# Kernel optimization log

Hardware: AMD Instinct MI355X
Metric: run time of the kernel (lower is better)

The kernel has to match this reference:

```python
import jax, jax.numpy as jnp
import numpy as np


def _conv2d(x, w, b, padding):
    # x: [N,C,H,W], w: [O,I,kh,kw]
    y = jax.lax.conv_general_dilated(
        x, w, window_strides=(1, 1), padding=padding,
        dimension_numbers=("NCHW", "OIHW", "NCHW"))
    return y + b[None, :, None, None]


def setup_inputs() -> dict:
    key = jax.random.key(0)
    ks = jax.random.split(key, 9)
    s = 0.05
    return {
        "x": jax.random.normal(ks[0], (16, 4, 512, 512), dtype=jnp.float32),
        "w1": jax.random.normal(ks[1], (32, 4, 3, 3), dtype=jnp.float32) * s,
        "b1": jax.random.normal(ks[2], (32,), dtype=jnp.float32) * s,
        "w2": jax.random.normal(ks[3], (4, 32, 3, 3), dtype=jnp.float32) * s,
        "b2": jax.random.normal(ks[4], (4,), dtype=jnp.float32) * s,
        "w_se1": jax.random.normal(ks[5], (16, 32, 1, 1), dtype=jnp.float32) * s,
        "b_se1": jax.random.normal(ks[6], (16,), dtype=jnp.float32) * s,
        "w_se2": jax.random.normal(ks[7], (32, 16, 1, 1), dtype=jnp.float32) * s,
        "b_se2": jax.random.normal(ks[8], (32,), dtype=jnp.float32) * s,
    }


def reference(x, w1, b1, w2, b2, w_se1, b_se1, w_se2, b_se2):
    x1 = x
    # module1: 3x3 conv (4->32) + ReLU
    h = jax.nn.relu(_conv2d(x, w1, b1, padding="SAME"))  # [N,32,H,W]
    se_in = h
    # SE branch: global avg pool -> 1x1 conv -> ReLU -> 1x1 conv -> sigmoid
    p = jnp.mean(h, axis=(2, 3), keepdims=True)  # [N,32,1,1]
    p = jax.nn.relu(_conv2d(p, w_se1, b_se1, padding="VALID"))  # [N,16,1,1]
    p = jax.nn.sigmoid(_conv2d(p, w_se2, b_se2, padding="VALID"))  # [N,32,1,1]
    h = p * se_in  # broadcast channel scaling
    # module2: 3x3 conv (32->4) + ReLU
    h = jax.nn.relu(_conv2d(h, w2, b2, padding="SAME"))  # [N,4,H,W]
    return h * x1  # residual multiply
```

## Files before the change

kernel.cpp:

```cpp
#include <hip/hip_runtime.h>
#include <math.h>

#define IMG 512

typedef __attribute__((ext_vector_type(4))) short short4_t;
typedef __attribute__((ext_vector_type(8))) short short8;
typedef __attribute__((ext_vector_type(4))) float f32x4;
typedef __attribute__((ext_vector_type(16))) float f32x16;
typedef __attribute__((ext_vector_type(2))) unsigned int u32x2;

__device__ __forceinline__ unsigned short f2bf(float f) {
  unsigned u = __builtin_bit_cast(unsigned, f);
  u += 0x7FFFu + ((u >> 16) & 1u);
  return (unsigned short)(u >> 16);
}
__device__ __forceinline__ unsigned cvtpk(float lo, float hi) {
  unsigned r;
  asm("v_cvt_pk_bf16_f32 %0, %1, %2" : "=v"(r) : "v"(lo), "v"(hi));
  return r;
}

__global__ __launch_bounds__(256) void k_prep(const float* __restrict__ w1,
                                              unsigned short* __restrict__ w1f) {
  const int t = threadIdx.x;
  if (t < 192) {
    const int kk = t >> 6, lane = t & 63;
    const int oc = lane & 31, hi = lane >> 5;
#pragma unroll
    for (int j = 0; j < 8; ++j) {
      const int dxp = 2 * hi + (j >> 2), ic = j & 3;
      float v = (dxp < 3) ? w1[((oc * 4 + ic) * 3 + kk) * 3 + dxp] : 0.f;
      w1f[(kk * 64 + lane) * 8 + j] = f2bf(v);
    }
  }
}

__global__ __launch_bounds__(256, 3) void k_pool(
    const float* __restrict__ x, const unsigned short* __restrict__ w1f,
    const float* __restrict__ b1, float* __restrict__ red_out, int use_atomic) {
  __shared__ unsigned short xs[34 * 40 * 4];
  __shared__ float pools[4][2][16];
  const int bid = blockIdx.x;
  const int swz = (bid & 7) * 512 + (bid >> 3);
  const int bx = swz & 15, by = (swz >> 4) & 15, n = swz >> 8;
  const int x0 = bx * 32, y0 = by * 32;
  const int t = threadIdx.x, lane = t & 63, wv = t >> 6;
  const int hi = lane >> 5;

  short8 A1[3];
#pragma unroll
  for (int kk = 0; kk < 3; ++kk)
    A1[kk] = *(const short8*)&w1f[(kk * 64 + lane) * 8];
  float bias_r[16];
#pragma unroll
  for (int r = 0; r < 16; ++r) {
    float bl = b1[(r & 3) + 8 * (r >> 2)], bh = b1[(r & 3) + 8 * (r >> 2) + 4];
    bias_r[r] = hi ? bh : bl;
  }

  const int sx = x0 - 4;
  const long CS = (long)IMG * IMG;
  for (int i = t; i < 340; i += 256) {
    const int row = i / 10, cb = i % 10;
    const int gy = y0 - 1 + row, gx0 = sx + cb * 4;
    f32x4 v0 = {0.f, 0.f, 0.f, 0.f}, v1 = v0, v2 = v0, v3 = v0;
    if (gy >= 0 && gy < IMG && gx0 >= 0 && gx0 < IMG) {
      const float* p = x + (((long)(n * 4) * IMG + gy) * IMG + gx0);
      v0 = *(const f32x4*)p;
      v1 = *(const f32x4*)(p + CS);
      v2 = *(const f32x4*)(p + 2 * CS);
      v3 = *(const f32x4*)(p + 3 * CS);
    }
    unsigned short* d = &xs[(row * 40 + cb * 4) * 4];
#pragma unroll
    for (int j = 0; j < 4; ++j) {
      u32x2 w;
      w[0] = cvtpk(v0[j], v1[j]);
      w[1] = cvtpk(v2[j], v3[j]);
      *(u32x2*)(d + j * 4) = w;
    }
  }
  __syncthreads();

  float pacc[16];
#pragma unroll
  for (int r = 0; r < 16; ++r) pacc[r] = 0.f;
  const int cx0 = (lane & 31) + 2 * hi + 3;
  const unsigned short* pP = &xs[((wv * 8) * 40 + cx0) * 4];
#define LOADP(K)                                                              \
  __builtin_shufflevector(*(const short4_t*)(pP + (K)*160),                   \
                          *(const short4_t*)(pP + (K)*160 + 4), 0, 1, 2, 3,   \
                          4, 5, 6, 7)
  short8 Ba, Bb, Bc;
  Ba = LOADP(0);
  Bb = LOADP(1);
#define P_ITER(IT, B0, B1, B2)                                                \
  {                                                                           \
    B2 = LOADP((IT) + 2);                                                     \
    f32x16 C;                                                                 \
    _Pragma("unroll") for (int r = 0; r < 16; ++r) C[r] = bias_r[r];          \
    C = __builtin_amdgcn_mfma_f32_32x32x16_bf16(A1[0], B0, C, 0, 0, 0);       \
    C = __builtin_amdgcn_mfma_f32_32x32x16_bf16(A1[1], B1, C, 0, 0, 0);       \
    C = __builtin_amdgcn_mfma_f32_32x32x16_bf16(A1[2], B2, C, 0, 0, 0);       \
    _Pragma("unroll") for (int r = 0; r < 16; ++r)                            \
        pacc[r] += fmaxf(C[r], 0.f);                                          \
  }
  P_ITER(0, Ba, Bb, Bc)
  P_ITER(1, Bb, Bc, Ba)
  P_ITER(2, Bc, Ba, Bb)
  P_ITER(3, Ba, Bb, Bc)
  P_ITER(4, Bb, Bc, Ba)
  P_ITER(5, Bc, Ba, Bb)
  P_ITER(6, Ba, Bb, Bc)
  P_ITER(7, Bb, Bc, Ba)
#undef P_ITER
#undef LOADP
#pragma unroll
  for (int r = 0; r < 16; ++r) {
#pragma unroll
    for (int m = 1; m < 32; m <<= 1) pacc[r] += __shfl_xor(pacc[r], m);
  }
  if ((lane & 31) == 0) {
#pragma unroll
    for (int r = 0; r < 16; ++r) pools[wv][hi][r] = pacc[r];
  }
  __syncthreads();
  if (t < 32) {
    const int c = t;
    const int hic = (c >> 2) & 1, reg = (c & 3) + 4 * (c >> 3);
    float s = pools[0][hic][reg] + pools[1][hic][reg] + pools[2][hic][reg] +
              pools[3][hic][reg];
    if (use_atomic) {
      atomicAdd(&red_out[n * 32 + c], s);
    } else {
      red_out[(n * 256 + by * 16 + bx) * 32 + c] = s;
    }
  }
}

__global__ __launch_bounds__(256) void k_se(
    const float* __restrict__ partials, const float* __restrict__ sums,
    const float* __restrict__ w_se1, const float* __restrict__ b_se1,
    const float* __restrict__ w_se2, const float* __restrict__ b_se2,
    const float* __restrict__ w2, unsigned short* __restrict__ w2f, int det) {
  const int n = blockIdx.x, t = threadIdx.x;
  __shared__ float red[8][32];
  __shared__ float mean_s[32], f1[16], p[32];
  if (det) {
    const int c = t & 31, s = t >> 5;
    float a = 0.f;
    for (int i = s * 32; i < s * 32 + 32; ++i)
      a += partials[(n * 256 + i) * 32 + c];
    red[s][c] = a;
    __syncthreads();
    if (t < 32) {
      float v = 0.f;
#pragma unroll
      for (int s2 = 0; s2 < 8; ++s2) v += red[s2][t];
      mean_s[t] = v * (1.0f / (512.f * 512.f));
    }
  } else {
    if (t < 32) mean_s[t] = sums[n * 32 + t] * (1.0f / (512.f * 512.f));
  }
  __syncthreads();
  if (t < 16) {
    float a = b_se1[t];
#pragma unroll
    for (int c = 0; c < 32; ++c) a += w_se1[t * 32 + c] * mean_s[c];
    f1[t] = fmaxf(a, 0.f);
  }
  __syncthreads();
  if (t < 32) {
    float a = b_se2[t];
#pragma unroll
    for (int c = 0; c < 16; ++c) a += w_se2[t * 16 + c] * f1[c];
    p[t] = 1.f / (1.f + expf(-a));
  }
  __syncthreads();
  for (int i = t; i < 9216; i += 256) {
    const int s = i >> 9, rem = i & 511, lane2 = rem >> 3, j = rem & 7;
    const int oc = lane2 & 3, yo = (lane2 >> 2) & 3, cg = lane2 >> 4;
    const int c = cg * 8 + j;
    const int dyy = s / 3, dx = s - dyy * 3, dy = dyy - yo;
    float v = 0.f;
    if (dy >= 0 && dy < 3) v = w2[(oc * 32 + c) * 9 + dy * 3 + dx] * p[c];
    w2f[((n * 18 + s) * 64 + lane2) * 8 + j] = f2bf(v);
  }
}

__global__ __launch_bounds__(256, 3) void k_main(
    const float* __restrict__ x, const unsigned short* __restrict__ w1f,
    const float* __restrict__ b1, const unsigned short* __restrict__ w2f,
    const float* __restrict__ b2, float* __restrict__ out) {
  __shared__ unsigned short xs[20 * 40 * 4];
  __shared__ unsigned short hs[18 * 32 * 32];
  const int bid = blockIdx.x;
  const int swz = (bid & 7) * 1152 + (bid >> 3);
  const int bx = swz % 18;
  const int q = swz / 18;
  const int by = q & 31, n = q >> 5;
  const int x0 = bx * 30, y0 = by * 16;
  const int t = threadIdx.x, lane = t & 63, wv = t >> 6;
  const int hi = lane >> 5;

  short8 A1[3];
#pragma unroll
  for (int kk = 0; kk < 3; ++kk)
    A1[kk] = *(const short8*)&w1f[(kk * 64 + lane) * 8];
  float bias_r[16];
#pragma unroll
  for (int r = 0; r < 16; ++r) {
    float bl = b1[(r & 3) + 8 * (r >> 2)], bh = b1[(r & 3) + 8 * (r >> 2) + 4];
    bias_r[r] = hi ? bh : bl;
  }

  const int sx = (x0 - 4) & ~3;
  const long CS = (long)IMG * IMG;
  for (int i = t; i < 200; i += 256) {
    const int row = i / 10, cb = i % 10;
    const int gy = y0 - 2 + row, gx0 = sx + cb * 4;
    f32x4 v0 = {0.f, 0.f, 0.f, 0.f}, v1 = v0, v2 = v0, v3 = v0;
    if (gy >= 0 && gy < IMG && gx0 >= 0 && gx0 < IMG) {
      const float* p = x + (((long)(n * 4) * IMG + gy) * IMG + gx0);
      v0 = *(const f32x4*)p;
      v1 = *(const f32x4*)(p + CS);
      v2 = *(const f32x4*)(p + 2 * CS);
      v3 = *(const f32x4*)(p + 3 * CS);
    }
    unsigned short* d = &xs[(row * 40 + cb * 4) * 4];
#pragma unroll
    for (int j = 0; j < 4; ++j) {
      u32x2 w;
      w[0] = cvtpk(v0[j], v1[j]);
      w[1] = cvtpk(v2[j], v3[j]);
      *(u32x2*)(d + j * 4) = w;
    }
  }
  __syncthreads();

  {
    const int px = lane & 31;
    const int cx0 = px + 2 * hi + (x0 - 2 - sx);
    const int q2 = (px >> 1) & 3;
    const int gxc = x0 - 1 + px;
    const bool colok = (gxc >= 0) && (gxc < IMG);
    const bool col_int = (x0 >= 1) && (x0 + 30 < IMG);
    const int R0 = (wv < 2) ? wv * 5 : 10 + (wv - 2) * 4;
    const unsigned short* pR = &xs[(R0 * 40 + cx0) * 4];
#define LOADX(K)                                                              \
  __builtin_shufflevector(*(const short4_t*)(pR + (K)*160),                   \
                          *(const short4_t*)(pR + (K)*160 + 4), 0, 1, 2, 3,   \
                          4, 5, 6, 7)
    short8 Ba, Bb, Bc;
    Ba = LOADX(0);
    Bb = LOADX(1);
#define C1_ITER(IT, B0, B1, B2)                                               \
  {                                                                           \
    B2 = LOADX((IT) + 2);                                                     \
    const int hy = R0 + (IT);                                                 \
    const int yi = y0 - 1 + hy;                                               \
    const bool row_ok = (yi >= 0) && (yi < IMG);                              \
    f32x16 C;                                                                 \
    _Pragma("unroll") for (int r = 0; r < 16; ++r) C[r] = bias_r[r];          \
    C = __builtin_amdgcn_mfma_f32_32x32x16_bf16(A1[0], B0, C, 0, 0, 0);       \
    C = __builtin_amdgcn_mfma_f32_32x32x16_bf16(A1[1], B1, C, 0, 0, 0);       \
    C = __builtin_amdgcn_mfma_f32_32x32x16_bf16(A1[2], B2, C, 0, 0, 0);       \
    const int usb = hy * 1024 + px * 32 + (hi << 2);                          \
    if (row_ok && col_int) {                                                  \
      _Pragma("unroll") for (int g = 0; g < 4; ++g) {                         \
        u32x2 w;                                                              \
        w[0] = cvtpk(fmaxf(C[4 * g + 0], 0.f), fmaxf(C[4 * g + 1], 0.f));     \
        w[1] = cvtpk(fmaxf(C[4 * g + 2], 0.f), fmaxf(C[4 * g + 3], 0.f));     \
        *(u32x2*)&hs[usb + ((g ^ q2) << 3)] = w;                              \
      }                                                                       \
    } else if (row_ok) {                                                      \
      _Pragma("unroll") for (int g = 0; g < 4; ++g) {                         \
        unsigned p01 =                                                        \
            cvtpk(fmaxf(C[4 * g + 0], 0.f), fmaxf(C[4 * g + 1], 0.f));        \
        unsigned p23 =                                                        \
            cvtpk(fmaxf(C[4 * g + 2], 0.f), fmaxf(C[4 * g + 3], 0.f));        \
        u32x2 w;                                                              \
        w[0] = colok ? p01 : 0u;                                              \
        w[1] = colok ? p23 : 0u;                                              \
        *(u32x2*)&hs[usb + ((g ^ q2) << 3)] = w;                              \
      }                                                                       \
    } else {                                                                  \
      u32x2 z;                                                                \
      z[0] = 0u;                                                              \
      z[1] = 0u;                                                              \
      _Pragma("unroll") for (int g = 0; g < 4; ++g)                           \
          *(u32x2*)&hs[usb + ((g ^ q2) << 3)] = z;                            \
    }                                                                         \
  }
    C1_ITER(0, Ba, Bb, Bc)
    C1_ITER(1, Bb, Bc, Ba)
    C1_ITER(2, Bc, Ba, Bb)
    C1_ITER(3, Ba, Bb, Bc)
    if (wv < 2) C1_ITER(4, Bb, Bc, Ba)
#undef C1_ITER
#undef LOADX
  }

  const unsigned short* w2b = w2f + (size_t)n * 9216 + lane * 8;
  short8 A2_0 = *(const short8*)(w2b + 0 * 512);
  short8 A2_1 = *(const short8*)(w2b + 1 * 512);
  short8 A2_2 = *(const short8*)(w2b + 2 * 512);
  short8 A2_3 = *(const short8*)(w2b + 3 * 512);
  short8 A2_4 = *(const short8*)(w2b + 4 * 512);
  short8 A2_5 = *(const short8*)(w2b + 5 * 512);
  short8 A2_6 = *(const short8*)(w2b + 6 * 512);
  short8 A2_7 = *(const short8*)(w2b + 7 * 512);
  short8 A2_8 = *(const short8*)(w2b + 8 * 512);
  short8 A2_9 = *(const short8*)(w2b + 9 * 512);
  short8 A2_10 = *(const short8*)(w2b + 10 * 512);
  short8 A2_11 = *(const short8*)(w2b + 11 * 512);
  short8 A2_12 = *(const short8*)(w2b + 12 * 512);
  short8 A2_13 = *(const short8*)(w2b + 13 * 512);
  short8 A2_14 = *(const short8*)(w2b + 14 * 512);
  short8 A2_15 = *(const short8*)(w2b + 15 * 512);
  short8 A2_16 = *(const short8*)(w2b + 16 * 512);
  short8 A2_17 = *(const short8*)(w2b + 17 * 512);
  asm volatile("" ::"v"(A2_0), "v"(A2_1), "v"(A2_2), "v"(A2_3), "v"(A2_4),
               "v"(A2_5), "v"(A2_6), "v"(A2_7), "v"(A2_8), "v"(A2_9),
               "v"(A2_10), "v"(A2_11), "v"(A2_12), "v"(A2_13), "v"(A2_14),
               "v"(A2_15), "v"(A2_16), "v"(A2_17));
  __syncthreads();

  {
    const int px16 = lane & 15, cg = lane >> 4;
    const int grp = wv & 1, ybq = wv >> 1;
    const int ox = grp * 16 + px16;
    const int yo = lane >> 4;
    const int gxo = x0 + ox;
    const bool epi_ok = (ox < 30) && (gxo < IMG);
    const float b20 = b2[0], b21 = b2[1], b22 = b2[2], b23 = b2[3];
    const int n4 = n * 4;
    int ph0 = ox + 0, ph1 = ox + 1, ph2 = ox + 2;
    ph2 = ph2 < 31 ? ph2 : 31;
    ph1 = ph1 < 31 ? ph1 : 31;
    const int ba0 = ph0 * 64 + ((cg ^ ((ph0 >> 1) & 3)) << 4);
    const int ba1 = ph1 * 64 + ((cg ^ ((ph1 >> 1) & 3)) << 4);
    const int ba2 = ph2 * 64 + ((cg ^ ((ph2 >> 1) & 3)) << 4);
    const char* hb = (const char*)hs + (ybq * 8) * 2048;
    f32x4 CA = {b20, b21, b22, b23};
    f32x4 CB = {b20, b21, b22, b23};
    short8 F0, F1, F2;

#define LOADF(R)                                                              \
  F0 = *(const short8*)(hb + (R)*2048 + ba0);                                 \
  F1 = *(const short8*)(hb + (R)*2048 + ba1);                                 \
  F2 = *(const short8*)(hb + (R)*2048 + ba2);
#define MFA(S0, S1, S2)                                                       \
  CA = __builtin_amdgcn_mfma_f32_16x16x32_bf16(A2_##S0, F0, CA, 0, 0, 0);     \
  CA = __builtin_amdgcn_mfma_f32_16x16x32_bf16(A2_##S1, F1, CA, 0, 0, 0);     \
  CA = __builtin_amdgcn_mfma_f32_16x16x32_bf16(A2_##S2, F2, CA, 0, 0, 0);
#define MFB(S0, S1, S2)                                                       \
  CB = __builtin_amdgcn_mfma_f32_16x16x32_bf16(A2_##S0, F0, CB, 0, 0, 0);     \
  CB = __builtin_amdgcn_mfma_f32_16x16x32_bf16(A2_##S1, F1, CB, 0, 0, 0);     \
  CB = __builtin_amdgcn_mfma_f32_16x16x32_bf16(A2_##S2, F2, CB, 0, 0, 0);

    __builtin_amdgcn_s_setprio(1);
    LOADF(0) MFA(0, 1, 2)
    LOADF(1) MFA(3, 4, 5)
    LOADF(2) MFA(6, 7, 8)
    LOADF(3) MFA(9, 10, 11)
    LOADF(4) MFA(12, 13, 14) MFB(0, 1, 2)
    LOADF(5) MFA(15, 16, 17) MFB(3, 4, 5)
    LOADF(6) MFB(6, 7, 8)
    LOADF(7) MFB(9, 10, 11)
    LOADF(8) MFB(12, 13, 14)
    LOADF(9) MFB(15, 16, 17)
    __builtin_amdgcn_s_setprio(0);
#undef LOADF
#undef MFA
#undef MFB

#define EPI2(CV, YB)                                                          \
  if (epi_ok) {                                                               \
    const int gy = y0 + (YB) + yo;                                            \
    const long i0 = ((long)n4 * IMG + gy) * IMG + gxo;                        \
    out[i0] = fmaxf(CV[0], 0.f) * x[i0];                                      \
    out[i0 + CS] = fmaxf(CV[1], 0.f) * x[i0 + CS];                            \
    out[i0 + 2 * CS] = fmaxf(CV[2], 0.f) * x[i0 + 2 * CS];                    \
    out[i0 + 3 * CS] = fmaxf(CV[3], 0.f) * x[i0 + 3 * CS];                    \
  }
    EPI2(CA, ybq * 8)
    EPI2(CB, ybq * 8 + 4)
#undef EPI2
  }
}

extern "C" void kernel_launch(void* const* d_in, const int* in_sizes, int n_in,
                              void* d_out, int out_size, void* d_ws,
                              size_t ws_size, hipStream_t stream) {
  const float* x = (const float*)d_in[0];
  const float* w1 = (const float*)d_in[1];
  const float* b1 = (const float*)d_in[2];
  const float* w2 = (const float*)d_in[3];
  const float* b2 = (const float*)d_in[4];
  const float* w_se1 = (const float*)d_in[5];
  const float* b_se1 = (const float*)d_in[6];
  const float* w_se2 = (const float*)d_in[7];
  const float* b_se2 = (const float*)d_in[8];
  float* out = (float*)d_out;
  float* ws = (float*)d_ws;

  float* sums = ws;
  unsigned short* w1f = (unsigned short*)(ws + 512);
  unsigned short* w2f = w1f + 1536;
  float* partials = (float*)(w2f + 147456);
  const size_t need_full =
      512 * 4 + 1536 * 2 + (size_t)147456 * 2 + (size_t)131072 * 4;

  k_prep<<<1, 256, 0, stream>>>(w1, w1f);
  if (ws_size >= need_full) {
    k_pool<<<4096, 256, 0, stream>>>(x, w1f, b1, partials, 0);
    k_se<<<16, 256, 0, stream>>>(partials, sums, w_se1, b_se1, w_se2, b_se2,
                                 w2, w2f, 1);
  } else {
    hipMemsetAsync(sums, 0, 512 * sizeof(float), stream);
    k_pool<<<4096, 256, 0, stream>>>(x, w1f, b1, sums, 1);
    k_se<<<16, 256, 0, stream>>>(partials, sums, w_se1, b_se1, w_se2, b_se2,
                                 w2, w2f, 0);
  }
  k_main<<<9216, 256, 0, stream>>>(x, w1f, b1, w2f, b2, out);
}
```

Baseline: 102.5 us.

## Process four row tiles per block with double-buffered input staging

Each block of the main fused conv kernel now walks four consecutive 16-row tiles instead of one, and the grid shrinks fourfold. The per-sample conv2 weights and the conv1 weights and biases are loaded once per block and reused across tiles. The x tile for the next rows is loaded into registers while conv1 runs on the current tile, then written to a second LDS buffer, so global load latency overlaps compute. The cost is more LDS (two staging buffers), extra barriers per tile, and fewer blocks to spread across CUs, which may lower occupancy or leave the load unbalanced.

```diff
diff --git a/kernel.cpp b/kernel.cpp
--- a/kernel.cpp
+++ b/kernel.cpp
@@ -8,6 +8,7 @@
 typedef __attribute__((ext_vector_type(4))) float f32x4;
 typedef __attribute__((ext_vector_type(16))) float f32x16;
 typedef __attribute__((ext_vector_type(2))) unsigned int u32x2;
+typedef __attribute__((ext_vector_type(4))) unsigned int u32x4;
 
 __device__ __forceinline__ unsigned short f2bf(float f) {
   unsigned u = __builtin_bit_cast(unsigned, f);
@@ -192,16 +193,43 @@
     const float* __restrict__ x, const unsigned short* __restrict__ w1f,
     const float* __restrict__ b1, const unsigned short* __restrict__ w2f,
     const float* __restrict__ b2, float* __restrict__ out) {
-  __shared__ unsigned short xs[20 * 40 * 4];
+  __shared__ unsigned short xs[2][20 * 40 * 4];
   __shared__ unsigned short hs[18 * 32 * 32];
   const int bid = blockIdx.x;
-  const int swz = (bid & 7) * 1152 + (bid >> 3);
+  const int swz = (bid & 7) * 288 + (bid >> 3);
   const int bx = swz % 18;
   const int q = swz / 18;
-  const int by = q & 31, n = q >> 5;
-  const int x0 = bx * 30, y0 = by * 16;
+  const int byq = q & 7, n = q >> 3;
+  const int x0 = bx * 30;
+  const int ybase = byq * 64;
   const int t = threadIdx.x, lane = t & 63, wv = t >> 6;
   const int hi = lane >> 5;
+  const int n4 = n * 4;
+  const long CS = (long)IMG * IMG;
+
+  const unsigned short* w2b = w2f + (size_t)n * 9216 + lane * 8;
+  short8 A2_0 = *(const short8*)(w2b + 0 * 512);
+  short8 A2_1 = *(const short8*)(w2b + 1 * 512);
+  short8 A2_2 = *(const short8*)(w2b + 2 * 512);
+  short8 A2_3 = *(const short8*)(w2b + 3 * 512);
+  short8 A2_4 = *(const short8*)(w2b + 4 * 512);
+  short8 A2_5 = *(const short8*)(w2b + 5 * 512);
+  short8 A2_6 = *(const short8*)(w2b + 6 * 512);
+  short8 A2_7 = *(const short8*)(w2b + 7 * 512);
+  short8 A2_8 = *(const short8*)(w2b + 8 * 512);
+  short8 A2_9 = *(const short8*)(w2b + 9 * 512);
+  short8 A2_10 = *(const short8*)(w2b + 10 * 512);
+  short8 A2_11 = *(const short8*)(w2b + 11 * 512);
+  short8 A2_12 = *(const short8*)(w2b + 12 * 512);
+  short8 A2_13 = *(const short8*)(w2b + 13 * 512);
+  short8 A2_14 = *(const short8*)(w2b + 14 * 512);
+  short8 A2_15 = *(const short8*)(w2b + 15 * 512);
+  short8 A2_16 = *(const short8*)(w2b + 16 * 512);
+  short8 A2_17 = *(const short8*)(w2b + 17 * 512);
+  asm volatile("" ::"v"(A2_0), "v"(A2_1), "v"(A2_2), "v"(A2_3), "v"(A2_4),
+               "v"(A2_5), "v"(A2_6), "v"(A2_7), "v"(A2_8), "v"(A2_9),
+               "v"(A2_10), "v"(A2_11), "v"(A2_12), "v"(A2_13), "v"(A2_14),
+               "v"(A2_15), "v"(A2_16), "v"(A2_17));
 
   short8 A1[3];
 #pragma unroll
@@ -215,38 +243,47 @@
   }
 
   const int sx = (x0 - 4) & ~3;
-  const long CS = (long)IMG * IMG;
-  for (int i = t; i < 200; i += 256) {
-    const int row = i / 10, cb = i % 10;
-    const int gy = y0 - 2 + row, gx0 = sx + cb * 4;
-    f32x4 v0 = {0.f, 0.f, 0.f, 0.f}, v1 = v0, v2 = v0, v3 = v0;
-    if (gy >= 0 && gy < IMG && gx0 >= 0 && gx0 < IMG) {
-      const float* p = x + (((long)(n * 4) * IMG + gy) * IMG + gx0);
-      v0 = *(const f32x4*)p;
-      v1 = *(const f32x4*)(p + CS);
-      v2 = *(const f32x4*)(p + 2 * CS);
-      v3 = *(const f32x4*)(p + 3 * CS);
-    }
-    unsigned short* d = &xs[(row * 40 + cb * 4) * 4];
-#pragma unroll
-    for (int j = 0; j < 4; ++j) {
-      u32x2 w;
-      w[0] = cvtpk(v0[j], v1[j]);
-      w[1] = cvtpk(v2[j], v3[j]);
-      *(u32x2*)(d + j * 4) = w;
-    }
-  }
-  __syncthreads();
-
-  {
-    const int px = lane & 31;
-    const int cx0 = px + 2 * hi + (x0 - 2 - sx);
-    const int q2 = (px >> 1) & 3;
-    const int gxc = x0 - 1 + px;
-    const bool colok = (gxc >= 0) && (gxc < IMG);
-    const bool col_int = (x0 >= 1) && (x0 + 30 < IMG);
-    const int R0 = (wv < 2) ? wv * 5 : 10 + (wv - 2) * 4;
-    const unsigned short* pR = &xs[(R0 * 40 + cx0) * 4];
+  const int srow = t / 10, cb = t % 10;
+  const int gxs = sx + cb * 4;
+  const bool scol = (t < 200) && (gxs >= 0) && (gxs < IMG);
+  const f32x4 zf = {0.f, 0.f, 0.f, 0.f};
+  f32x4 sv0 = zf, sv1 = zf, sv2 = zf, sv3 = zf;
+
+  auto stage_issue = [&](int ytile) {
+    const int gy = ytile - 2 + srow;
+    if (scol && gy >= 0 && gy < IMG) {
+      const float* p = x + (((long)n4 * IMG + gy) * IMG + gxs);
+      sv0 = *(const f32x4*)p;
+      sv1 = *(const f32x4*)(p + CS);
+      sv2 = *(const f32x4*)(p + 2 * CS);
+      sv3 = *(const f32x4*)(p + 3 * CS);
+    } else {
+      sv0 = zf; sv1 = zf; sv2 = zf; sv3 = zf;
+    }
+  };
+  auto stage_write = [&](unsigned short* xbuf) {
+    if (t < 200) {
+      unsigned short* d = &xbuf[(srow * 40 + cb * 4) * 4];
+      u32x4 w0, w1;
+      w0[0] = cvtpk(sv0[0], sv1[0]); w0[1] = cvtpk(sv2[0], sv3[0]);
+      w0[2] = cvtpk(sv0[1], sv1[1]); w0[3] = cvtpk(sv2[1], sv3[1]);
+      w1[0] = cvtpk(sv0[2], sv1[2]); w1[1] = cvtpk(sv2[2], sv3[2]);
+      w1[2] = cvtpk(sv0[3], sv1[3]); w1[3] = cvtpk(sv2[3], sv3[3]);
+      *(u32x4*)d = w0;
+      *(u32x4*)(d + 8) = w1;
+    }
+  };
+
+  const int px = lane & 31;
+  const int cx0 = px + 2 * hi + (x0 - 2 - sx);
+  const int q2 = (px >> 1) & 3;
+  const int gxc = x0 - 1 + px;
+  const bool colok = (gxc >= 0) && (gxc < IMG);
+  const bool col_int = (x0 >= 1) && (x0 + 30 < IMG);
+  const int R0 = (wv < 2) ? wv * 5 : 10 + (wv - 2) * 4;
+
+  auto conv1_tile = [&](const unsigned short* xbuf, int ytile) {
+    const unsigned short* pR = &xbuf[(R0 * 40 + cx0) * 4];
 #define LOADX(K)                                                              \
   __builtin_shufflevector(*(const short4_t*)(pR + (K)*160),                   \
                           *(const short4_t*)(pR + (K)*160 + 4), 0, 1, 2, 3,   \
@@ -258,7 +295,7 @@
   {                                                                           \
     B2 = LOADX((IT) + 2);                                                     \
     const int hy = R0 + (IT);                                                 \
-    const int yi = y0 - 1 + hy;                                               \
+    const int yi = ytile - 1 + hy;                                            \
     const bool row_ok = (yi >= 0) && (yi < IMG);                              \
     f32x16 C;                                                                 \
     _Pragma("unroll") for (int r = 0; r < 16; ++r) C[r] = bias_r[r];          \
@@ -299,53 +336,27 @@
     if (wv < 2) C1_ITER(4, Bb, Bc, Ba)
 #undef C1_ITER
 #undef LOADX
-  }
-
-  const unsigned short* w2b = w2f + (size_t)n * 9216 + lane * 8;
-  short8 A2_0 = *(const short8*)(w2b + 0 * 512);
-  short8 A2_1 = *(const short8*)(w2b + 1 * 512);
-  short8 A2_2 = *(const short8*)(w2b + 2 * 512);
-  short8 A2_3 = *(const short8*)(w2b + 3 * 512);
-  short8 A2_4 = *(const short8*)(w2b + 4 * 512);
-  short8 A2_5 = *(const short8*)(w2b + 5 * 512);
-  short8 A2_6 = *(const short8*)(w2b + 6 * 512);
-  short8 A2_7 = *(const short8*)(w2b + 7 * 512);
-  short8 A2_8 = *(const short8*)(w2b + 8 * 512);
-  short8 A2_9 = *(const short8*)(w2b + 9 * 512);
-  short8 A2_10 = *(const short8*)(w2b + 10 * 512);
-  short8 A2_11 = *(const short8*)(w2b + 11 * 512);
-  short8 A2_12 = *(const short8*)(w2b + 12 * 512);
-  short8 A2_13 = *(const short8*)(w2b + 13 * 512);
-  short8 A2_14 = *(const short8*)(w2b + 14 * 512);
-  short8 A2_15 = *(const short8*)(w2b + 15 * 512);
-  short8 A2_16 = *(const short8*)(w2b + 16 * 512);
-  short8 A2_17 = *(const short8*)(w2b + 17 * 512);
-  asm volatile("" ::"v"(A2_0), "v"(A2_1), "v"(A2_2), "v"(A2_3), "v"(A2_4),
-               "v"(A2_5), "v"(A2_6), "v"(A2_7), "v"(A2_8), "v"(A2_9),
-               "v"(A2_10), "v"(A2_11), "v"(A2_12), "v"(A2_13), "v"(A2_14),
-               "v"(A2_15), "v"(A2_16), "v"(A2_17));
-  __syncthreads();
-
-  {
-    const int px16 = lane & 15, cg = lane >> 4;
-    const int grp = wv & 1, ybq = wv >> 1;
-    const int ox = grp * 16 + px16;
-    const int yo = lane >> 4;
-    const int gxo = x0 + ox;
-    const bool epi_ok = (ox < 30) && (gxo < IMG);
-    const float b20 = b2[0], b21 = b2[1], b22 = b2[2], b23 = b2[3];
-    const int n4 = n * 4;
-    int ph0 = ox + 0, ph1 = ox + 1, ph2 = ox + 2;
-    ph2 = ph2 < 31 ? ph2 : 31;
-    ph1 = ph1 < 31 ? ph1 : 31;
-    const int ba0 = ph0 * 64 + ((cg ^ ((ph0 >> 1) & 3)) << 4);
-    const int ba1 = ph1 * 64 + ((cg ^ ((ph1 >> 1) & 3)) << 4);
-    const int ba2 = ph2 * 64 + ((cg ^ ((ph2 >> 1) & 3)) << 4);
-    const char* hb = (const char*)hs + (ybq * 8) * 2048;
+  };
+
+  const int px16 = lane & 15, cg = lane >> 4;
+  const int grp = wv & 1, wrow = wv >> 1;
+  const int ox = grp * 16 + px16;
+  const int yo = lane >> 4;
+  const int gxo = x0 + ox;
+  const bool epi_ok = (ox < 30) && (gxo < IMG);
+  const float b20 = b2[0], b21 = b2[1], b22 = b2[2], b23 = b2[3];
+  int ph0 = ox, ph1 = ox + 1, ph2 = ox + 2;
+  ph2 = ph2 < 31 ? ph2 : 31;
+  ph1 = ph1 < 31 ? ph1 : 31;
+  const int ba0 = ph0 * 64 + ((cg ^ ((ph0 >> 1) & 3)) << 4);
+  const int ba1 = ph1 * 64 + ((cg ^ ((ph1 >> 1) & 3)) << 4);
+  const int ba2 = ph2 * 64 + ((cg ^ ((ph2 >> 1) & 3)) << 4);
+  const char* hb = (const char*)hs + (wrow * 8) * 2048;
+
+  auto conv2_tile = [&](int ytile) {
     f32x4 CA = {b20, b21, b22, b23};
     f32x4 CB = {b20, b21, b22, b23};
     short8 F0, F1, F2;
-
 #define LOADF(R)                                                              \
   F0 = *(const short8*)(hb + (R)*2048 + ba0);                                 \
   F1 = *(const short8*)(hb + (R)*2048 + ba1);                                 \
@@ -358,7 +369,6 @@
   CB = __builtin_amdgcn_mfma_f32_16x16x32_bf16(A2_##S0, F0, CB, 0, 0, 0);     \
   CB = __builtin_amdgcn_mfma_f32_16x16x32_bf16(A2_##S1, F1, CB, 0, 0, 0);     \
   CB = __builtin_amdgcn_mfma_f32_16x16x32_bf16(A2_##S2, F2, CB, 0, 0, 0);
-
     __builtin_amdgcn_s_setprio(1);
     LOADF(0) MFA(0, 1, 2)
     LOADF(1) MFA(3, 4, 5)
@@ -374,19 +384,32 @@
 #undef LOADF
 #undef MFA
 #undef MFB
-
 #define EPI2(CV, YB)                                                          \
   if (epi_ok) {                                                               \
-    const int gy = y0 + (YB) + yo;                                            \
+    const int gy = ytile + (YB) + yo;                                         \
     const long i0 = ((long)n4 * IMG + gy) * IMG + gxo;                        \
     out[i0] = fmaxf(CV[0], 0.f) * x[i0];                                      \
     out[i0 + CS] = fmaxf(CV[1], 0.f) * x[i0 + CS];                            \
     out[i0 + 2 * CS] = fmaxf(CV[2], 0.f) * x[i0 + 2 * CS];                    \
     out[i0 + 3 * CS] = fmaxf(CV[3], 0.f) * x[i0 + 3 * CS];                    \
   }
-    EPI2(CA, ybq * 8)
-    EPI2(CB, ybq * 8 + 4)
+    EPI2(CA, wrow * 8)
+    EPI2(CB, wrow * 8 + 4)
 #undef EPI2
+  };
+
+  stage_issue(ybase);
+  stage_write(xs[0]);
+  __syncthreads();
+
+#pragma unroll
+  for (int ti = 0; ti < 4; ++ti) {
+    if (ti < 3) stage_issue(ybase + (ti + 1) * 16);
+    conv1_tile(xs[ti & 1], ybase + ti * 16);
+    __syncthreads();
+    if (ti < 3) stage_write(xs[(ti + 1) & 1]);
+    conv2_tile(ybase + ti * 16);
+    if (ti < 3) __syncthreads();
   }
 }
 
@@ -423,5 +446,5 @@
     k_se<<<16, 256, 0, stream>>>(partials, sums, w_se1, b_se1, w_se2, b_se2,
                                  w2, w2f, 0);
   }
-  k_main<<<9216, 256, 0, stream>>>(x, w1f, b1, w2f, b2, out);
-}
+  k_main<<<2304, 256, 0, stream>>>(x, w1f, b1, w2f, b2, out);
+}
```

Result: slower. 134.1 us (+30.8%).

## Halve k_main row tile to 8 rows and raise occupancy to five blocks

Applied to the files above, without the earlier changes.

The main fused conv kernel now processes 8 output rows per block instead of 16, doubling the grid size and shrinking the shared-memory buffers for the input and hidden tiles. The second conv accumulates into one output fragment per wave instead of two, and its weights are loaded from global memory inside the MFMA sequence rather than preloaded into 18 register vectors. Launch bounds rise from 3 to 5 blocks per CU to raise occupancy. In exchange, the halo overhead grows: each block computes 10 hidden rows for 8 output rows instead of 18 for 16, so more conv1 work and more input loads are duplicated.

```diff
diff --git a/kernel.cpp b/kernel.cpp
--- a/kernel.cpp
+++ b/kernel.cpp
@@ -188,20 +188,21 @@
   }
 }
 
-__global__ __launch_bounds__(256, 3) void k_main(
+__global__ __launch_bounds__(256, 5) void k_main(
     const float* __restrict__ x, const unsigned short* __restrict__ w1f,
     const float* __restrict__ b1, const unsigned short* __restrict__ w2f,
     const float* __restrict__ b2, float* __restrict__ out) {
-  __shared__ unsigned short xs[20 * 40 * 4];
-  __shared__ unsigned short hs[18 * 32 * 32];
+  __shared__ unsigned short xs[12 * 40 * 4];
+  __shared__ unsigned short hs[10 * 32 * 32];
   const int bid = blockIdx.x;
-  const int swz = (bid & 7) * 1152 + (bid >> 3);
+  const int swz = (bid & 7) * 2304 + (bid >> 3);
   const int bx = swz % 18;
   const int q = swz / 18;
-  const int by = q & 31, n = q >> 5;
-  const int x0 = bx * 30, y0 = by * 16;
+  const int by = q & 63, n = q >> 6;
+  const int x0 = bx * 30, ytile = by * 8;
   const int t = threadIdx.x, lane = t & 63, wv = t >> 6;
   const int hi = lane >> 5;
+  const long CS = (long)IMG * IMG;
 
   short8 A1[3];
 #pragma unroll
@@ -215,10 +216,9 @@
   }
 
   const int sx = (x0 - 4) & ~3;
-  const long CS = (long)IMG * IMG;
-  for (int i = t; i < 200; i += 256) {
-    const int row = i / 10, cb = i % 10;
-    const int gy = y0 - 2 + row, gx0 = sx + cb * 4;
+  if (t < 120) {
+    const int row = t / 10, cb = t % 10;
+    const int gy = ytile - 2 + row, gx0 = sx + cb * 4;
     f32x4 v0 = {0.f, 0.f, 0.f, 0.f}, v1 = v0, v2 = v0, v3 = v0;
     if (gy >= 0 && gy < IMG && gx0 >= 0 && gx0 < IMG) {
       const float* p = x + (((long)(n * 4) * IMG + gy) * IMG + gx0);
@@ -245,7 +245,7 @@
     const int gxc = x0 - 1 + px;
     const bool colok = (gxc >= 0) && (gxc < IMG);
     const bool col_int = (x0 >= 1) && (x0 + 30 < IMG);
-    const int R0 = (wv < 2) ? wv * 5 : 10 + (wv - 2) * 4;
+    const int R0 = (wv < 2) ? 3 * wv : 6 + 2 * (wv - 2);
     const unsigned short* pR = &xs[(R0 * 40 + cx0) * 4];
 #define LOADX(K)                                                              \
   __builtin_shufflevector(*(const short4_t*)(pR + (K)*160),                   \
@@ -258,7 +258,7 @@
   {                                                                           \
     B2 = LOADX((IT) + 2);                                                     \
     const int hy = R0 + (IT);                                                 \
-    const int yi = y0 - 1 + hy;                                               \
+    const int yi = ytile - 1 + hy;                                            \
     const bool row_ok = (yi >= 0) && (yi < IMG);                              \
     f32x16 C;                                                                 \
     _Pragma("unroll") for (int r = 0; r < 16; ++r) C[r] = bias_r[r];          \
@@ -294,99 +294,61 @@
   }
     C1_ITER(0, Ba, Bb, Bc)
     C1_ITER(1, Bb, Bc, Ba)
-    C1_ITER(2, Bc, Ba, Bb)
-    C1_ITER(3, Ba, Bb, Bc)
-    if (wv < 2) C1_ITER(4, Bb, Bc, Ba)
+    if (wv < 2) C1_ITER(2, Bc, Ba, Bb)
 #undef C1_ITER
 #undef LOADX
   }
-
-  const unsigned short* w2b = w2f + (size_t)n * 9216 + lane * 8;
-  short8 A2_0 = *(const short8*)(w2b + 0 * 512);
-  short8 A2_1 = *(const short8*)(w2b + 1 * 512);
-  short8 A2_2 = *(const short8*)(w2b + 2 * 512);
-  short8 A2_3 = *(const short8*)(w2b + 3 * 512);
-  short8 A2_4 = *(const short8*)(w2b + 4 * 512);
-  short8 A2_5 = *(const short8*)(w2b + 5 * 512);
-  short8 A2_6 = *(const short8*)(w2b + 6 * 512);
-  short8 A2_7 = *(const short8*)(w2b + 7 * 512);
-  short8 A2_8 = *(const short8*)(w2b + 8 * 512);
-  short8 A2_9 = *(const short8*)(w2b + 9 * 512);
-  short8 A2_10 = *(const short8*)(w2b + 10 * 512);
-  short8 A2_11 = *(const short8*)(w2b + 11 * 512);
-  short8 A2_12 = *(const short8*)(w2b + 12 * 512);
-  short8 A2_13 = *(const short8*)(w2b + 13 * 512);
-  short8 A2_14 = *(const short8*)(w2b + 14 * 512);
-  short8 A2_15 = *(const short8*)(w2b + 15 * 512);
-  short8 A2_16 = *(const short8*)(w2b + 16 * 512);
-  short8 A2_17 = *(const short8*)(w2b + 17 * 512);
-  asm volatile("" ::"v"(A2_0), "v"(A2_1), "v"(A2_2), "v"(A2_3), "v"(A2_4),
-               "v"(A2_5), "v"(A2_6), "v"(A2_7), "v"(A2_8), "v"(A2_9),
-               "v"(A2_10), "v"(A2_11), "v"(A2_12), "v"(A2_13), "v"(A2_14),
-               "v"(A2_15), "v"(A2_16), "v"(A2_17));
   __syncthreads();
 
   {
     const int px16 = lane & 15, cg = lane >> 4;
-    const int grp = wv & 1, ybq = wv >> 1;
+    const int grp = wv & 1, wrow = wv >> 1;
     const int ox = grp * 16 + px16;
     const int yo = lane >> 4;
     const int gxo = x0 + ox;
     const bool epi_ok = (ox < 30) && (gxo < IMG);
     const float b20 = b2[0], b21 = b2[1], b22 = b2[2], b23 = b2[3];
-    const int n4 = n * 4;
-    int ph0 = ox + 0, ph1 = ox + 1, ph2 = ox + 2;
+    int ph0 = ox, ph1 = ox + 1, ph2 = ox + 2;
     ph2 = ph2 < 31 ? ph2 : 31;
     ph1 = ph1 < 31 ? ph1 : 31;
     const int ba0 = ph0 * 64 + ((cg ^ ((ph0 >> 1) & 3)) << 4);
     const int ba1 = ph1 * 64 + ((cg ^ ((ph1 >> 1) & 3)) << 4);
     const int ba2 = ph2 * 64 + ((cg ^ ((ph2 >> 1) & 3)) << 4);
-    const char* hb = (const char*)hs + (ybq * 8) * 2048;
+    const char* hb = (const char*)hs + (wrow * 4) * 2048;
+    const unsigned short* w2b = w2f + (size_t)n * 9216 + lane * 8;
     f32x4 CA = {b20, b21, b22, b23};
-    f32x4 CB = {b20, b21, b22, b23};
     short8 F0, F1, F2;
 
+#define A2F(S) (*(const short8*)(w2b + (S)*512))
 #define LOADF(R)                                                              \
   F0 = *(const short8*)(hb + (R)*2048 + ba0);                                 \
   F1 = *(const short8*)(hb + (R)*2048 + ba1);                                 \
   F2 = *(const short8*)(hb + (R)*2048 + ba2);
 #define MFA(S0, S1, S2)                                                       \
-  CA = __builtin_amdgcn_mfma_f32_16x16x32_bf16(A2_##S0, F0, CA, 0, 0, 0);     \
-  CA = __builtin_amdgcn_mfma_f32_16x16x32_bf16(A2_##S1, F1, CA, 0, 0, 0);     \
-  CA = __builtin_amdgcn_mfma_f32_16x16x32_bf16(A2_##S2, F2, CA, 0, 0, 0);
-#define MFB(S0, S1, S2)                                                       \
-  CB = __builtin_amdgcn_mfma_f32_16x16x32_bf16(A2_##S0, F0, CB, 0, 0, 0);     \
-  CB = __builtin_amdgcn_mfma_f32_16x16x32_bf16(A2_##S1, F1, CB, 0, 0, 0);     \
-  CB = __builtin_amdgcn_mfma_f32_16x16x32_bf16(A2_##S2, F2, CB, 0, 0, 0);
+  CA = __builtin_amdgcn_mfma_f32_16x16x32_bf16(A2F(S0), F0, CA, 0, 0, 0);     \
+  CA = __builtin_amdgcn_mfma_f32_16x16x32_bf16(A2F(S1), F1, CA, 0, 0, 0);     \
+  CA = __builtin_amdgcn_mfma_f32_16x16x32_bf16(A2F(S2), F2, CA, 0, 0, 0);
 
     __builtin_amdgcn_s_setprio(1);
     LOADF(0) MFA(0, 1, 2)
     LOADF(1) MFA(3, 4, 5)
     LOADF(2) MFA(6, 7, 8)
     LOADF(3) MFA(9, 10, 11)
-    LOADF(4) MFA(12, 13, 14) MFB(0, 1, 2)
-    LOADF(5) MFA(15, 16, 17) MFB(3, 4, 5)
-    LOADF(6) MFB(6, 7, 8)
-    LOADF(7) MFB(9, 10, 11)
-    LOADF(8) MFB(12, 13, 14)
-    LOADF(9) MFB(15, 16, 17)
+    LOADF(4) MFA(12, 13, 14)
+    LOADF(5) MFA(15, 16, 17)
     __builtin_amdgcn_s_setprio(0);
 #undef LOADF
 #undef MFA
-#undef MFB
-
-#define EPI2(CV, YB)                                                          \
-  if (epi_ok) {                                                               \
-    const int gy = y0 + (YB) + yo;                                            \
-    const long i0 = ((long)n4 * IMG + gy) * IMG + gxo;                        \
-    out[i0] = fmaxf(CV[0], 0.f) * x[i0];                                      \
-    out[i0 + CS] = fmaxf(CV[1], 0.f) * x[i0 + CS];                            \
-    out[i0 + 2 * CS] = fmaxf(CV[2], 0.f) * x[i0 + 2 * CS];                    \
-    out[i0 + 3 * CS] = fmaxf(CV[3], 0.f) * x[i0 + 3 * CS];                    \
-  }
-    EPI2(CA, ybq * 8)
-    EPI2(CB, ybq * 8 + 4)
-#undef EPI2
+#undef A2F
+
+    if (epi_ok) {
+      const int gy = ytile + wrow * 4 + yo;
+      const long i0 = ((long)(n * 4) * IMG + gy) * IMG + gxo;
+      out[i0] = fmaxf(CA[0], 0.f) * x[i0];
+      out[i0 + CS] = fmaxf(CA[1], 0.f) * x[i0 + CS];
+      out[i0 + 2 * CS] = fmaxf(CA[2], 0.f) * x[i0 + 2 * CS];
+      out[i0 + 3 * CS] = fmaxf(CA[3], 0.f) * x[i0 + 3 * CS];
+    }
   }
 }
 
@@ -423,5 +385,5 @@
     k_se<<<16, 256, 0, stream>>>(partials, sums, w_se1, b_se1, w_se2, b_se2,
                                  w2, w2f, 0);
   }
-  k_main<<<9216, 256, 0, stream>>>(x, w1f, b1, w2f, b2, out);
-}
+  k_main<<<18432, 256, 0, stream>>>(x, w1f, b1, w2f, b2, out);
+}
```

Result: slower. 113.1 us (+10.3%).

## Enlarge pooling tiles to 64x64, fold w1 prep into kernels, widen LDS stores

Applied to the files above, without the earlier changes.

Removes the separate w1 prep kernel launch. Each kernel now builds its bf16 A1 fragments directly from the fp32 weights with packed converts. The pooling kernel tile grows from 32x32 to 64x64, with 1024 blocks instead of 4096, and each wave loops over four row groups. Fewer blocks cut halo reloads and per-block setup and shrink the partial-sum buffer read by the SE kernel. The larger LDS tile and the occupancy hint raised to 4 may limit residency, and every block now redoes the weight conversion.

```diff
diff --git a/kernel.cpp b/kernel.cpp
--- a/kernel.cpp
+++ b/kernel.cpp
@@ -8,6 +8,7 @@
 typedef __attribute__((ext_vector_type(4))) float f32x4;
 typedef __attribute__((ext_vector_type(16))) float f32x16;
 typedef __attribute__((ext_vector_type(2))) unsigned int u32x2;
+typedef __attribute__((ext_vector_type(4))) unsigned int u32x4;
 
 __device__ __forceinline__ unsigned short f2bf(float f) {
   unsigned u = __builtin_bit_cast(unsigned, f);
@@ -20,37 +21,40 @@
   return r;
 }
 
-__global__ __launch_bounds__(256) void k_prep(const float* __restrict__ w1,
-                                              unsigned short* __restrict__ w1f) {
-  const int t = threadIdx.x;
-  if (t < 192) {
-    const int kk = t >> 6, lane = t & 63;
-    const int oc = lane & 31, hi = lane >> 5;
+__device__ __forceinline__ void load_A1(const float* __restrict__ w1,
+                                        int lane, short8 A1[3]) {
+  const int oc = lane & 31, hi = lane >> 5;
+#pragma unroll
+  for (int kk = 0; kk < 3; ++kk) {
+    float v[8];
 #pragma unroll
     for (int j = 0; j < 8; ++j) {
       const int dxp = 2 * hi + (j >> 2), ic = j & 3;
-      float v = (dxp < 3) ? w1[((oc * 4 + ic) * 3 + kk) * 3 + dxp] : 0.f;
-      w1f[(kk * 64 + lane) * 8 + j] = f2bf(v);
-    }
-  }
-}
-
-__global__ __launch_bounds__(256, 3) void k_pool(
-    const float* __restrict__ x, const unsigned short* __restrict__ w1f,
+      v[j] = (dxp < 3) ? w1[((oc * 4 + ic) * 3 + kk) * 3 + dxp] : 0.f;
+    }
+    u32x4 u;
+    u[0] = cvtpk(v[0], v[1]);
+    u[1] = cvtpk(v[2], v[3]);
+    u[2] = cvtpk(v[4], v[5]);
+    u[3] = cvtpk(v[6], v[7]);
+    A1[kk] = __builtin_bit_cast(short8, u);
+  }
+}
+
+__global__ __launch_bounds__(256, 4) void k_pool(
+    const float* __restrict__ x, const float* __restrict__ w1,
     const float* __restrict__ b1, float* __restrict__ red_out, int use_atomic) {
-  __shared__ unsigned short xs[34 * 40 * 4];
+  __shared__ unsigned short xs[66 * 72 * 4];
   __shared__ float pools[4][2][16];
   const int bid = blockIdx.x;
-  const int swz = (bid & 7) * 512 + (bid >> 3);
-  const int bx = swz & 15, by = (swz >> 4) & 15, n = swz >> 8;
-  const int x0 = bx * 32, y0 = by * 32;
+  const int swz = (bid & 7) * 128 + (bid >> 3);
+  const int bx = swz & 7, by = (swz >> 3) & 7, n = swz >> 6;
+  const int x0 = bx * 64, y0 = by * 64;
   const int t = threadIdx.x, lane = t & 63, wv = t >> 6;
   const int hi = lane >> 5;
 
   short8 A1[3];
-#pragma unroll
-  for (int kk = 0; kk < 3; ++kk)
-    A1[kk] = *(const short8*)&w1f[(kk * 64 + lane) * 8];
+  load_A1(w1, lane, A1);
   float bias_r[16];
 #pragma unroll
   for (int r = 0; r < 16; ++r) {
@@ -60,8 +64,8 @@
 
   const int sx = x0 - 4;
   const long CS = (long)IMG * IMG;
-  for (int i = t; i < 340; i += 256) {
-    const int row = i / 10, cb = i % 10;
+  for (int i = t; i < 66 * 18; i += 256) {
+    const int row = i / 18, cb = i % 18;
     const int gy = y0 - 1 + row, gx0 = sx + cb * 4;
     f32x4 v0 = {0.f, 0.f, 0.f, 0.f}, v1 = v0, v2 = v0, v3 = v0;
     if (gy >= 0 && gy < IMG && gx0 >= 0 && gx0 < IMG) {
@@ -71,29 +75,37 @@
       v2 = *(const f32x4*)(p + 2 * CS);
       v3 = *(const f32x4*)(p + 3 * CS);
     }
-    unsigned short* d = &xs[(row * 40 + cb * 4) * 4];
-#pragma unroll
-    for (int j = 0; j < 4; ++j) {
-      u32x2 w;
-      w[0] = cvtpk(v0[j], v1[j]);
-      w[1] = cvtpk(v2[j], v3[j]);
-      *(u32x2*)(d + j * 4) = w;
-    }
+    unsigned short* d = &xs[(row * 72 + cb * 4) * 4];
+    u32x4 wa, wb;
+    wa[0] = cvtpk(v0[0], v1[0]);
+    wa[1] = cvtpk(v2[0], v3[0]);
+    wa[2] = cvtpk(v0[1], v1[1]);
+    wa[3] = cvtpk(v2[1], v3[1]);
+    wb[0] = cvtpk(v0[2], v1[2]);
+    wb[1] = cvtpk(v2[2], v3[2]);
+    wb[2] = cvtpk(v0[3], v1[3]);
+    wb[3] = cvtpk(v2[3], v3[3]);
+    *(u32x4*)d = wa;
+    *(u32x4*)(d + 8) = wb;
   }
   __syncthreads();
 
   float pacc[16];
 #pragma unroll
   for (int r = 0; r < 16; ++r) pacc[r] = 0.f;
-  const int cx0 = (lane & 31) + 2 * hi + 3;
-  const unsigned short* pP = &xs[((wv * 8) * 40 + cx0) * 4];
+  const int half = wv & 1;
+  const int cx0 = (lane & 31) + half * 32 + 2 * hi + 3;
+#pragma unroll
+  for (int k = 0; k < 4; ++k) {
+    const int rg = (wv >> 1) + 2 * k;
+    const unsigned short* pP = &xs[((rg * 8) * 72 + cx0) * 4];
 #define LOADP(K)                                                              \
-  __builtin_shufflevector(*(const short4_t*)(pP + (K)*160),                   \
-                          *(const short4_t*)(pP + (K)*160 + 4), 0, 1, 2, 3,   \
+  __builtin_shufflevector(*(const short4_t*)(pP + (K)*288),                   \
+                          *(const short4_t*)(pP + (K)*288 + 4), 0, 1, 2, 3,   \
                           4, 5, 6, 7)
-  short8 Ba, Bb, Bc;
-  Ba = LOADP(0);
-  Bb = LOADP(1);
+    short8 Ba, Bb, Bc;
+    Ba = LOADP(0);
+    Bb = LOADP(1);
 #define P_ITER(IT, B0, B1, B2)                                                \
   {                                                                           \
     B2 = LOADP((IT) + 2);                                                     \
@@ -105,16 +117,17 @@
     _Pragma("unroll") for (int r = 0; r < 16; ++r)                            \
         pacc[r] += fmaxf(C[r], 0.f);                                          \
   }
-  P_ITER(0, Ba, Bb, Bc)
-  P_ITER(1, Bb, Bc, Ba)
-  P_ITER(2, Bc, Ba, Bb)
-  P_ITER(3, Ba, Bb, Bc)
-  P_ITER(4, Bb, Bc, Ba)
-  P_ITER(5, Bc, Ba, Bb)
-  P_ITER(6, Ba, Bb, Bc)
-  P_ITER(7, Bb, Bc, Ba)
+    P_ITER(0, Ba, Bb, Bc)
+    P_ITER(1, Bb, Bc, Ba)
+    P_ITER(2, Bc, Ba, Bb)
+    P_ITER(3, Ba, Bb, Bc)
+    P_ITER(4, Bb, Bc, Ba)
+    P_ITER(5, Bc, Ba, Bb)
+    P_ITER(6, Ba, Bb, Bc)
+    P_ITER(7, Bb, Bc, Ba)
 #undef P_ITER
 #undef LOADP
+  }
 #pragma unroll
   for (int r = 0; r < 16; ++r) {
 #pragma unroll
@@ -133,7 +146,7 @@
     if (use_atomic) {
       atomicAdd(&red_out[n * 32 + c], s);
     } else {
-      red_out[(n * 256 + by * 16 + bx) * 32 + c] = s;
+      red_out[(n * 64 + by * 8 + bx) * 32 + c] = s;
     }
   }
 }
@@ -149,8 +162,8 @@
   if (det) {
     const int c = t & 31, s = t >> 5;
     float a = 0.f;
-    for (int i = s * 32; i < s * 32 + 32; ++i)
-      a += partials[(n * 256 + i) * 32 + c];
+    for (int i = s * 8; i < s * 8 + 8; ++i)
+      a += partials[(n * 64 + i) * 32 + c];
     red[s][c] = a;
     __syncthreads();
     if (t < 32) {
@@ -189,7 +202,7 @@
 }
 
 __global__ __launch_bounds__(256, 3) void k_main(
-    const float* __restrict__ x, const unsigned short* __restrict__ w1f,
+    const float* __restrict__ x, const float* __restrict__ w1,
     const float* __restrict__ b1, const unsigned short* __restrict__ w2f,
     const float* __restrict__ b2, float* __restrict__ out) {
   __shared__ unsigned short xs[20 * 40 * 4];
@@ -204,9 +217,7 @@
   const int hi = lane >> 5;
 
   short8 A1[3];
-#pragma unroll
-  for (int kk = 0; kk < 3; ++kk)
-    A1[kk] = *(const short8*)&w1f[(kk * 64 + lane) * 8];
+  load_A1(w1, lane, A1);
   float bias_r[16];
 #pragma unroll
   for (int r = 0; r < 16; ++r) {
@@ -335,7 +346,7 @@
     const bool epi_ok = (ox < 30) && (gxo < IMG);
     const float b20 = b2[0], b21 = b2[1], b22 = b2[2], b23 = b2[3];
     const int n4 = n * 4;
-    int ph0 = ox + 0, ph1 = ox + 1, ph2 = ox + 2;
+    int ph0 = ox, ph1 = ox + 1, ph2 = ox + 2;
     ph2 = ph2 < 31 ? ph2 : 31;
     ph1 = ph1 < 31 ? ph1 : 31;
     const int ba0 = ph0 * 64 + ((cg ^ ((ph0 >> 1) & 3)) << 4);
@@ -406,22 +417,20 @@
   float* ws = (float*)d_ws;
 
   float* sums = ws;
-  unsigned short* w1f = (unsigned short*)(ws + 512);
-  unsigned short* w2f = w1f + 1536;
+  unsigned short* w2f = (unsigned short*)(ws + 512);
   float* partials = (float*)(w2f + 147456);
   const size_t need_full =
-      512 * 4 + 1536 * 2 + (size_t)147456 * 2 + (size_t)131072 * 4;
-
-  k_prep<<<1, 256, 0, stream>>>(w1, w1f);
+      512 * 4 + (size_t)147456 * 2 + (size_t)32768 * 4;
+
   if (ws_size >= need_full) {
-    k_pool<<<4096, 256, 0, stream>>>(x, w1f, b1, partials, 0);
+    k_pool<<<1024, 256, 0, stream>>>(x, w1, b1, partials, 0);
     k_se<<<16, 256, 0, stream>>>(partials, sums, w_se1, b_se1, w_se2, b_se2,
                                  w2, w2f, 1);
   } else {
     hipMemsetAsync(sums, 0, 512 * sizeof(float), stream);
-    k_pool<<<4096, 256, 0, stream>>>(x, w1f, b1, sums, 1);
+    k_pool<<<1024, 256, 0, stream>>>(x, w1, b1, sums, 1);
     k_se<<<16, 256, 0, stream>>>(partials, sums, w_se1, b_se1, w_se2, b_se2,
                                  w2, w2f, 0);
   }
-  k_main<<<9216, 256, 0, stream>>>(x, w1f, b1, w2f, b2, out);
-}
+  k_main<<<9216, 256, 0, stream>>>(x, w1, b1, w2f, b2, out);
+}
```

Measured after the change: 192.1 us. 1.87x slower.
